# Optimization experiments

Hardware: AMD Instinct MI355X
Metric: run time of the kernel (lower is better)

## Reference

```python
import jax, jax.numpy as jnp
import numpy as np

N_STREAMS = 8
DIM = 1024
N_HEADS = 16
HEAD_DIM = DIM // N_HEADS
STREAM_DIM = DIM // N_STREAMS
EPS = 1e-6


def setup_inputs() -> dict:
    key = jax.random.key(0)
    ks = jax.random.split(key, 20)
    B, S, D = 2, 2048, DIM
    inp = {
        "x": jax.random.normal(ks[0], (B, S, D), jnp.float32),
        "rope_cos": jax.random.uniform(ks[1], (S, HEAD_DIM), jnp.float32),
        "rope_sin": jax.random.uniform(ks[2], (S, HEAD_DIM), jnp.float32),
        # DeltaOperator: learned per-channel decay logits
        "delta_decay": jax.random.normal(ks[3], (D,), jnp.float32) * 0.02,
        # gate_proj: Linear(D, 3*n)
        "gate_w": jax.random.normal(ks[4], (3 * N_STREAMS, D), jnp.float32) * 0.02,
        "gate_b": jnp.zeros((3 * N_STREAMS,), jnp.float32),
        "phi_res": jax.random.normal(ks[5], (N_STREAMS, N_STREAMS), jnp.float32) * 0.02,
        "ln1_w": jnp.ones((D,), jnp.float32),
        "ln2_w": jnp.ones((D,), jnp.float32),
        # MLP (StrategicLinear == Linear at inference)
        "w1": jax.random.normal(ks[6], (4 * D, D), jnp.float32) * 0.02,
        "b1": jnp.zeros((4 * D,), jnp.float32),
        "w2": jax.random.normal(ks[7], (D, 4 * D), jnp.float32) * 0.02,
        "b2": jnp.zeros((D,), jnp.float32),
        # nn.MultiheadAttention params
        "in_proj_w": jax.random.normal(ks[8], (3 * D, D), jnp.float32) * 0.02,
        "in_proj_b": jnp.zeros((3 * D,), jnp.float32),
        "out_w": jax.random.normal(ks[9], (D, D), jnp.float32) * 0.02,
        "out_b": jnp.zeros((D,), jnp.float32),
    }
    return inp


def delta_operator(x, decay_logits):
    # out_t = x_t - s_{t-1};  s_t = beta*s_{t-1} + (1-beta)*x_t  (per-channel EMA delta)
    beta = jax.nn.sigmoid(decay_logits)  # [D]

    def step(s, xt):
        out = xt - s
        s_new = beta * s + (1.0 - beta) * xt
        return s_new, out

    xT = jnp.swapaxes(x, 0, 1)  # [S,B,D]
    s0 = jnp.zeros_like(xT[0])
    _, ysT = jax.lax.scan(step, s0, xT)
    return jnp.swapaxes(ysT, 0, 1)  # [B,S,D]


def rms_norm(x, w):
    var = jnp.mean(x * x, axis=-1, keepdims=True)
    return x * jax.lax.rsqrt(var + EPS) * w


def sinkhorn_knopp(phi, iterations=15):
    K = jnp.exp(phi)
    for _ in range(iterations):
        K = K / jnp.sum(K, axis=1, keepdims=True)
        K = K / jnp.sum(K, axis=0, keepdims=True)
    return K


def causal_mha(x, in_proj_w, in_proj_b, out_w, out_b):
    B, S, D = x.shape
    qkv = x @ in_proj_w.T + in_proj_b  # [B,S,3D]
    q, k, v = jnp.split(qkv, 3, axis=-1)
    def heads(t):
        return t.reshape(B, S, N_HEADS, HEAD_DIM).transpose(0, 2, 1, 3)  # [B,H,S,hd]
    q, k, v = heads(q), heads(k), heads(v)
    scores = jnp.einsum("bhqd,bhkd->bhqk", q, k) / jnp.sqrt(jnp.float32(HEAD_DIM))
    mask = jnp.tril(jnp.ones((S, S), bool))
    scores = jnp.where(mask, scores, jnp.float32(-1e9))
    attn = jax.nn.softmax(scores, axis=-1)
    o = jnp.einsum("bhqk,bhkd->bhqd", attn, v)
    o = o.transpose(0, 2, 1, 3).reshape(B, S, D)
    return o @ out_w.T + out_b


def reference(x, rope_cos, rope_sin, delta_decay, gate_w, gate_b, phi_res,
              ln1_w, ln2_w, w1, b1, w2, b2, in_proj_w, in_proj_b, out_w, out_b):
    B, S, D = x.shape
    n = N_STREAMS
    x_delta = delta_operator(x, delta_decay)
    x_state = jnp.mean(x_delta, axis=1)  # [B,D]
    gates = x_state @ gate_w.T + gate_b  # [B,3n]
    g_res = jax.nn.sigmoid(gates[:, 2 * n:])[:, None, :, None]  # [B,1,n,1]
    H_res = sinkhorn_knopp(phi_res, 15)
    x_streams = x_delta.reshape(B, S, n, STREAM_DIM)
    # (x_perm @ H.T).permute back == einsum over stream axis
    mhc_out = jnp.einsum("bsnd,mn->bsmd", x_streams * g_res, H_res).reshape(B, S, D)
    normed = rms_norm(x_delta, ln1_w)
    attn_out = causal_mha(normed, in_proj_w, in_proj_b, out_w, out_b)
    normed2 = rms_norm(x_delta + attn_out, ln2_w)
    h = jax.nn.gelu(normed2 @ w1.T + b1, approximate=False)
    ffn_out = h @ w2.T + b2
    return x_delta + attn_out + ffn_out + mhc_out
```

## Files before the change

### kernel.cpp

```cpp
#include <hip/hip_runtime.h>
#include <hip/hip_bf16.h>
#include <math.h>

#define BB 2
#define SS 2048
#define DDIM 1024
#define NHEAD 16
#define NSTR 8
#define SDIMC 128
#define NCH 16
#define CLEN 128
#define EPSV 1e-6f

using bf16 = __hip_bfloat16;
typedef __attribute__((ext_vector_type(8))) __bf16 bf8;
typedef __attribute__((ext_vector_type(4))) __bf16 bf4v;
typedef __attribute__((ext_vector_type(4))) float f4;

__device__ __forceinline__ bf16 f2b(float v) { return __float2bfloat16(v); }
__device__ __forceinline__ bf8 ld8(const bf16* p) { return *(const bf8*)p; }
__device__ __forceinline__ f4 MFMA(bf8 a, bf8 b, f4 c) {
  return __builtin_amdgcn_mfma_f32_16x16x32_bf16(a, b, c, 0, 0, 0);
}
__device__ __forceinline__ float sigm(float x) { return 1.0f / (1.0f + expf(-x)); }
__device__ __forceinline__ float fexp2(float x) { return __builtin_amdgcn_exp2f(x); }
__device__ __forceinline__ float max3f(float a, float b, float c) {
  return fmaxf(fmaxf(a, b), c);
}

__device__ __forceinline__ float gelu_f(float v) {
  float x = v * 0.70710678118654752f;
  float ax = fabsf(x);
  float t = __builtin_amdgcn_rcpf(1.0f + 0.3275911f * ax);
  float p = ((((1.061405429f * t - 1.453152027f) * t + 1.421413741f) * t
              - 0.284496736f) * t + 0.254829592f) * t;
  float e = 1.0f - p * fexp2(-ax * ax * 1.4426950408889634f);
  e = copysignf(e, x);
  return 0.5f * v * (1.0f + e);
}

__device__ __forceinline__ void glds16(bf16* l, const bf16* g) {
  __builtin_amdgcn_global_load_lds(
      (const __attribute__((address_space(1))) unsigned int*)g,
      (__attribute__((address_space(3))) unsigned int*)l, 16, 0, 0);
}

__global__ __launch_bounds__(256) void cvt_all(const float* __restrict__ ipw,
                                               const float* __restrict__ ow,
                                               const float* __restrict__ w1,
                                               const float* __restrict__ w2,
                                               bf16* __restrict__ WIPW,
                                               bf16* __restrict__ WOW,
                                               bf16* __restrict__ W1B,
                                               bf16* __restrict__ W2B) {
  const int S1 = 3 * DDIM * DDIM, S2 = S1 + DDIM * DDIM,
            S3 = S2 + 4 * DDIM * DDIM;
  int i4 = (blockIdx.x * 256 + threadIdx.x) * 4;
  const float* src;
  bf16* dst;
  int off;
  if (i4 < S1)      { src = ipw; dst = WIPW; off = i4; }
  else if (i4 < S2) { src = ow;  dst = WOW;  off = i4 - S1; }
  else if (i4 < S3) { src = w1;  dst = W1B;  off = i4 - S2; }
  else              { src = w2;  dst = W2B;  off = i4 - S3; }
  float4 v = *(const float4*)(src + off);
  bf4v o;
  o[0] = (__bf16)v.x; o[1] = (__bf16)v.y; o[2] = (__bf16)v.z; o[3] = (__bf16)v.w;
  *(bf4v*)(dst + off) = o;
}

__global__ __launch_bounds__(256) void delta_passA(const float* __restrict__ x,
                                                   const float* __restrict__ decay,
                                                   float* __restrict__ SA) {
  int idx = blockIdx.x * 256 + threadIdx.x;
  int d = idx % DDIM;
  int c = (idx / DDIM) % NCH;
  int b = idx / (DDIM * NCH);
  float beta = sigm(decay[d]);
  float omb = 1.0f - beta;
  const float* xp = x + ((size_t)(b * SS + c * CLEN)) * DDIM + d;
  float s = 0.0f;
  for (int j = 0; j < CLEN; j++) {
    float xv = xp[(size_t)j * DDIM];
    s = beta * s + omb * xv;
  }
  SA[idx] = s;
}

__global__ __launch_bounds__(256) void delta_passB(const float* __restrict__ SA,
                                                   const float* __restrict__ decay,
                                                   float* __restrict__ SIN) {
  int idx = blockIdx.x * 256 + threadIdx.x;
  int d = idx % DDIM;
  int b = idx / DDIM;
  float beta = sigm(decay[d]);
  float p = beta;
  for (int i = 0; i < 7; i++) p *= p;
  float s = 0.0f;
  for (int c = 0; c < NCH; c++) {
    SIN[(b * NCH + c) * DDIM + d] = s;
    s = p * s + SA[(b * NCH + c) * DDIM + d];
  }
}

__global__ __launch_bounds__(256) void delta_passC(const float* __restrict__ x,
                                                   const float* __restrict__ decay,
                                                   const float* __restrict__ SIN,
                                                   float* __restrict__ XD,
                                                   float* __restrict__ SA) {
  int idx = blockIdx.x * 256 + threadIdx.x;
  int d = idx % DDIM;
  int c = (idx / DDIM) % NCH;
  int b = idx / (DDIM * NCH);
  float beta = sigm(decay[d]);
  float omb = 1.0f - beta;
  const float* xp = x + ((size_t)(b * SS + c * CLEN)) * DDIM + d;
  float* xdp = XD + ((size_t)(b * SS + c * CLEN)) * DDIM + d;
  float s = SIN[idx];
  float sum = 0.0f;
  for (int j = 0; j < CLEN; j++) {
    float xv = xp[(size_t)j * DDIM];
    float o = xv - s;
    xdp[(size_t)j * DDIM] = o;
    sum += o;
    s = beta * s + omb * xv;
  }
  SA[idx] = sum;
}

__global__ __launch_bounds__(1024) void gates_sinkhorn(const float* __restrict__ SA,
                                                       const float* __restrict__ gw,
                                                       const float* __restrict__ gb,
                                                       const float* __restrict__ phi,
                                                       float* __restrict__ gres,
                                                       float* __restrict__ hres) {
  int tid = threadIdx.x;
  int wave = tid >> 6, lane = tid & 63;
  int b = wave >> 3, j = wave & 7;
  float acc = 0.0f;
  for (int d = lane; d < DDIM; d += 64) {
    float xs = 0.0f;
    for (int c = 0; c < NCH; c++) xs += SA[(b * NCH + c) * DDIM + d];
    xs *= (1.0f / (float)SS);
    acc += xs * gw[(2 * NSTR + j) * DDIM + d];
  }
  for (int off = 32; off > 0; off >>= 1) acc += __shfl_down(acc, off);
  if (lane == 0) gres[b * NSTR + j] = sigm(acc + gb[2 * NSTR + j]);
  __syncthreads();
  if (tid == 0) {
    float Km[8][8];
    for (int i = 0; i < 8; i++)
      for (int jj = 0; jj < 8; jj++) Km[i][jj] = expf(phi[i * 8 + jj]);
    for (int it = 0; it < 15; it++) {
      for (int i = 0; i < 8; i++) {
        float rs = 0.0f;
        for (int jj = 0; jj < 8; jj++) rs += Km[i][jj];
        float inv = 1.0f / rs;
        for (int jj = 0; jj < 8; jj++) Km[i][jj] *= inv;
      }
      for (int jj = 0; jj < 8; jj++) {
        float cs = 0.0f;
        for (int i = 0; i < 8; i++) cs += Km[i][jj];
        float inv = 1.0f / cs;
        for (int i = 0; i < 8; i++) Km[i][jj] *= inv;
      }
    }
    for (int i = 0; i < 8; i++)
      for (int jj = 0; jj < 8; jj++) hres[i * 8 + jj] = Km[i][jj];
  }
}

__global__ __launch_bounds__(256) void rmsnorm_k(const float* __restrict__ in,
                                                 const float* __restrict__ w,
                                                 bf16* __restrict__ out) {
  int row = blockIdx.x;
  const float* r = in + (size_t)row * DDIM;
  int tid = threadIdx.x;
  float ss = 0.0f;
  for (int i = tid; i < DDIM; i += 256) {
    float v = r[i];
    ss += v * v;
  }
  for (int off = 32; off > 0; off >>= 1) ss += __shfl_down(ss, off);
  __shared__ float red[4];
  if ((tid & 63) == 0) red[tid >> 6] = ss;
  __syncthreads();
  float tot = red[0] + red[1] + red[2] + red[3];
  float sc = rsqrtf(tot / (float)DDIM + EPSV);
  bf16* o = out + (size_t)row * DDIM;
  for (int i = tid; i < DDIM; i += 256) o[i] = f2b(r[i] * sc * w[i]);
}

template <int EPI>
__global__ __launch_bounds__(512, 2) void gemm256(const bf16* __restrict__ Ag,
                                                  const bf16* __restrict__ Wg,
                                                  const float* __restrict__ bias,
                                                  bf16* __restrict__ outp,
                                                  int M, int N, int K, int nby) {
  __shared__ __align__(16) bf16 As[2][16384];
  __shared__ __align__(16) bf16 Bs[2][16384];
  int nwg = gridDim.x;
  int cpx = nwg >> 3;
  int l = (blockIdx.x & 7) * cpx + (blockIdx.x >> 3);
  int bm = l / nby, bn = l % nby;
  int m0 = bm * 256, n0 = bn * 256;
  int tid = threadIdx.x;
  int lane = tid & 63, wv = tid >> 6;
  int ml = lane & 15, quad = lane >> 4;
  int wrow = wv >> 2, wcol = wv & 3;

  size_t aoff[2][2], boff[2][2];
  int lof[2][2];
#pragma unroll
  for (int h = 0; h < 2; h++)
#pragma unroll
    for (int j = 0; j < 2; j++) {
      int b = tid * 16 + j * 8192;
      int s = b >> 10, w = b & 1023;
      int wl = w ^ (((w >> 9) & 1) << 5);
      int row = h * 128 + (s >> 1) * 16 + (wl >> 6);
      int col = (s & 1) * 32 + ((wl & 63) >> 1);
      aoff[h][j] = (size_t)(m0 + row) * K + col;
      boff[h][j] = (size_t)(n0 + row) * K + col;
      lof[h][j] = (h * 16384 + b) >> 1;
    }
  int wq2 = ((((ml << 6) + (quad << 4)) ^ (((int)(ml >= 8)) << 5))) >> 1;

#define SA_(c, kt, h) { glds16(&As[c][lof[h][0]], Ag + aoff[h][0] + (size_t)(kt) * 64); \
                        glds16(&As[c][lof[h][1]], Ag + aoff[h][1] + (size_t)(kt) * 64); }
#define SB_(c, kt, h) { glds16(&Bs[c][lof[h][0]], Wg + boff[h][0] + (size_t)(kt) * 64); \
                        glds16(&Bs[c][lof[h][1]], Wg + boff[h][1] + (size_t)(kt) * 64); }

  SA_(0, 0, 0); SA_(0, 0, 1);
  SB_(0, 0, 0); SB_(0, 0, 1);
  SB_(1, 1, 0); SB_(1, 1, 1);
  f4 acc[8][4] = {};
  asm volatile("s_waitcnt vmcnt(4)" ::: "memory");
  __builtin_amdgcn_s_barrier();
  asm volatile("" ::: "memory");

  int T = K >> 6;
  for (int t = 0; t < T; t++) {
    int c = t & 1;
    bf8 bfrag[4][2];
#pragma unroll
    for (int q = 0; q < 4; q++) {
      bf8 af[2][2];
#pragma unroll
      for (int mi2 = 0; mi2 < 2; mi2++)
#pragma unroll
        for (int kk = 0; kk < 2; kk++)
          af[mi2][kk] =
              ld8(&As[c][(((wrow * 8 + q * 2 + mi2) * 2 + kk) << 9) + wq2]);
      if (q == 0) {
#pragma unroll
        for (int ni = 0; ni < 4; ni++)
#pragma unroll
          for (int kk = 0; kk < 2; kk++)
            bfrag[ni][kk] =
                ld8(&Bs[c][(((wcol * 4 + ni) * 2 + kk) << 9) + wq2]);
      }
      if (q == 0 && t + 1 < T) SA_(c ^ 1, t + 1, 0);
      if (q == 1 && t + 1 < T) SA_(c ^ 1, t + 1, 1);
      if (q == 2 && t + 2 < T) SB_(c, t + 2, 0);
      if (q == 3 && t + 2 < T) SB_(c, t + 2, 1);
      __builtin_amdgcn_s_barrier();
      asm volatile("s_waitcnt lgkmcnt(0)" ::: "memory");
      __builtin_amdgcn_s_setprio(1);
#pragma unroll
      for (int mi2 = 0; mi2 < 2; mi2++)
#pragma unroll
        for (int ni = 0; ni < 4; ni++)
#pragma unroll
          for (int kk = 0; kk < 2; kk++)
            acc[q * 2 + mi2][ni] =
                MFMA(af[mi2][kk], bfrag[ni][kk], acc[q * 2 + mi2][ni]);
      __builtin_amdgcn_s_setprio(0);
      if (q == 3) {
        if (t + 2 < T) {
          asm volatile("s_waitcnt vmcnt(4)" ::: "memory");
        } else if (t + 1 < T) {
          asm volatile("s_waitcnt vmcnt(0)" ::: "memory");
        }
      }
      __builtin_amdgcn_s_barrier();
      asm volatile("" ::: "memory");
    }
  }
#pragma unroll
  for (int mi = 0; mi < 8; mi++)
#pragma unroll
    for (int ni = 0; ni < 4; ni++)
#pragma unroll
      for (int r = 0; r < 4; r++) {
        int row = m0 + wrow * 128 + mi * 16 + quad * 4 + r;
        int col = n0 + wcol * 64 + ni * 16 + ml;
        float v = acc[mi][ni][r] + bias[col];
        if (EPI == 1) v = gelu_f(v);
        outp[(size_t)row * N + col] = f2b(v);
      }
#undef SA_
#undef SB_
}

__global__ __launch_bounds__(512, 2) void gemm256sk(const bf16* __restrict__ Ag,
                                                    const bf16* __restrict__ Wg,
                                                    bf16* __restrict__ P01,
                                                    bf16* __restrict__ P23,
                                                    int M, int N, int K, int LDK,
                                                    int nby) {
  __shared__ __align__(16) bf16 As[2][16384];
  __shared__ __align__(16) bf16 Bs[2][16384];
  int nwg = gridDim.x;
  int cpx = nwg >> 3;
  int l = (blockIdx.x & 7) * cpx + (blockIdx.x >> 3);
  int nper = nwg >> 2;
  int sk = l / nper;
  int idx = l % nper;
  int bm = idx / nby, bn = idx % nby;
  int m0 = bm * 256, n0 = bn * 256;
  bf16* outp = (sk < 2) ? (P01 + (size_t)sk * M * N)
                        : (P23 + (size_t)(sk - 2) * M * N);
  int kbase = sk * K;
  int tid = threadIdx.x;
  int lane = tid & 63, wv = tid >> 6;
  int ml = lane & 15, quad = lane >> 4;
  int wrow = wv >> 2, wcol = wv & 3;

  size_t aoff[2][2], boff[2][2];
  int lof[2][2];
#pragma unroll
  for (int h = 0; h < 2; h++)
#pragma unroll
    for (int j = 0; j < 2; j++) {
      int b = tid * 16 + j * 8192;
      int s = b >> 10, w = b & 1023;
      int wl = w ^ (((w >> 9) & 1) << 5);
      int row = h * 128 + (s >> 1) * 16 + (wl >> 6);
      int col = (s & 1) * 32 + ((wl & 63) >> 1);
      aoff[h][j] = (size_t)(m0 + row) * LDK + kbase + col;
      boff[h][j] = (size_t)(n0 + row) * LDK + kbase + col;
      lof[h][j] = (h * 16384 + b) >> 1;
    }
  int wq2 = ((((ml << 6) + (quad << 4)) ^ (((int)(ml >= 8)) << 5))) >> 1;

#define SA_(c, kt, h) { glds16(&As[c][lof[h][0]], Ag + aoff[h][0] + (size_t)(kt) * 64); \
                        glds16(&As[c][lof[h][1]], Ag + aoff[h][1] + (size_t)(kt) * 64); }
#define SB_(c, kt, h) { glds16(&Bs[c][lof[h][0]], Wg + boff[h][0] + (size_t)(kt) * 64); \
                        glds16(&Bs[c][lof[h][1]], Wg + boff[h][1] + (size_t)(kt) * 64); }

  SA_(0, 0, 0); SA_(0, 0, 1);
  SB_(0, 0, 0); SB_(0, 0, 1);
  SB_(1, 1, 0); SB_(1, 1, 1);
  f4 acc[8][4] = {};
  asm volatile("s_waitcnt vmcnt(4)" ::: "memory");
  __builtin_amdgcn_s_barrier();
  asm volatile("" ::: "memory");

  int T = K >> 6;
  for (int t = 0; t < T; t++) {
    int c = t & 1;
    bf8 bfrag[4][2];
#pragma unroll
    for (int q = 0; q < 4; q++) {
      bf8 af[2][2];
#pragma unroll
      for (int mi2 = 0; mi2 < 2; mi2++)
#pragma unroll
        for (int kk = 0; kk < 2; kk++)
          af[mi2][kk] =
              ld8(&As[c][(((wrow * 8 + q * 2 + mi2) * 2 + kk) << 9) + wq2]);
      if (q == 0) {
#pragma unroll
        for (int ni = 0; ni < 4; ni++)
#pragma unroll
          for (int kk = 0; kk < 2; kk++)
            bfrag[ni][kk] =
                ld8(&Bs[c][(((wcol * 4 + ni) * 2 + kk) << 9) + wq2]);
      }
      if (q == 0 && t + 1 < T) SA_(c ^ 1, t + 1, 0);
      if (q == 1 && t + 1 < T) SA_(c ^ 1, t + 1, 1);
      if (q == 2 && t + 2 < T) SB_(c, t + 2, 0);
      if (q == 3 && t + 2 < T) SB_(c, t + 2, 1);
      __builtin_amdgcn_s_barrier();
      asm volatile("s_waitcnt lgkmcnt(0)" ::: "memory");
      __builtin_amdgcn_s_setprio(1);
#pragma unroll
      for (int mi2 = 0; mi2 < 2; mi2++)
#pragma unroll
        for (int ni = 0; ni < 4; ni++)
#pragma unroll
          for (int kk = 0; kk < 2; kk++)
            acc[q * 2 + mi2][ni] =
                MFMA(af[mi2][kk], bfrag[ni][kk], acc[q * 2 + mi2][ni]);
      __builtin_amdgcn_s_setprio(0);
      if (q == 3) {
        if (t + 2 < T) {
          asm volatile("s_waitcnt vmcnt(4)" ::: "memory");
        } else if (t + 1 < T) {
          asm volatile("s_waitcnt vmcnt(0)" ::: "memory");
        }
      }
      __builtin_amdgcn_s_barrier();
      asm volatile("" ::: "memory");
    }
  }
#pragma unroll
  for (int mi = 0; mi < 8; mi++)
#pragma unroll
    for (int ni = 0; ni < 4; ni++)
#pragma unroll
      for (int r = 0; r < 4; r++) {
        int row = m0 + wrow * 128 + mi * 16 + quad * 4 + r;
        int col = n0 + wcol * 64 + ni * 16 + ml;
        outp[(size_t)row * N + col] = f2b(acc[mi][ni][r]);
      }
#undef SA_
#undef SB_
}

template <int ODT, int EPI>
__global__ __launch_bounds__(256) void gemm_lds64(const bf16* __restrict__ A,
                                                  const bf16* __restrict__ W,
                                                  const float* __restrict__ bias,
                                                  const float* __restrict__ res,
                                                  void* __restrict__ outp,
                                                  int M, int N, int K) {
  __shared__ bf16 As[2][64 * 32];
  __shared__ bf16 Bs[2][128 * 32];
  int tid = threadIdx.x;
  int lane = tid & 63, wv = tid >> 6;
  int ml = lane & 15, quad = lane >> 4;
  int wr = wv & 1, wc = wv >> 1;
  int m0 = blockIdx.x * 64, n0 = blockIdx.y * 128;
  const bf16* gaA;
  const bf16* gb[2];
  int lofA, lofs[2];
  {
    int c = tid;
    int row = c >> 2, kc = (c & 3) * 8;
    gaA = A + (size_t)(m0 + row) * K + kc;
    lofA = c * 8;
  }
#pragma unroll
  for (int it = 0; it < 2; it++) {
    int c = it * 256 + tid;
    int row = c >> 2, kc = (c & 3) * 8;
    gb[it] = W + (size_t)(n0 + row) * K + kc;
    lofs[it] = c * 8;
  }
  glds16(&As[0][lofA], gaA);
#pragma unroll
  for (int it = 0; it < 2; it++) glds16(&Bs[0][lofs[it]], gb[it]);
  f4 acc[2][4] = {};
  int nk = K >> 5;
  int cur = 0;
  __syncthreads();
  for (int t = 0; t < nk; t++) {
    if (t + 1 < nk) {
      int ko = (t + 1) * 32;
      glds16(&As[cur ^ 1][lofA], gaA + ko);
#pragma unroll
      for (int it = 0; it < 2; it++) glds16(&Bs[cur ^ 1][lofs[it]], gb[it] + ko);
    }
    bf8 af[2], bfr[4];
#pragma unroll
    for (int mi = 0; mi < 2; mi++)
      af[mi] = ld8(&As[cur][(wr * 32 + mi * 16 + ml) * 32 + quad * 8]);
#pragma unroll
    for (int ni = 0; ni < 4; ni++)
      bfr[ni] = ld8(&Bs[cur][(wc * 64 + ni * 16 + ml) * 32 + quad * 8]);
#pragma unroll
    for (int mi = 0; mi < 2; mi++)
#pragma unroll
      for (int ni = 0; ni < 4; ni++)
        acc[mi][ni] = MFMA(af[mi], bfr[ni], acc[mi][ni]);
    __syncthreads();
    cur ^= 1;
  }
#pragma unroll
  for (int mi = 0; mi < 2; mi++)
#pragma unroll
    for (int ni = 0; ni < 4; ni++)
#pragma unroll
      for (int r = 0; r < 4; r++) {
        int row = m0 + wr * 32 + mi * 16 + quad * 4 + r;
        int col = n0 + wc * 64 + ni * 16 + ml;
        size_t idx = (size_t)row * N + col;
        float v = acc[mi][ni][r] + bias[col];
        if (EPI == 1) v = gelu_f(v);
        if (EPI == 2) v += res[idx];
        if (ODT == 1) ((bf16*)outp)[idx] = f2b(v);
        else ((float*)outp)[idx] = v;
      }
}

__global__ __launch_bounds__(256) void vtrans(const bf16* __restrict__ qkv,
                                              bf16* __restrict__ VT) {
  int bid = blockIdx.x;
  int st = bid % (SS / 64);
  int h = (bid / (SS / 64)) % NHEAD;
  int b = bid / ((SS / 64) * NHEAD);
  __shared__ bf16 tile[64][65];
  int s0 = st * 64;
  int tid = threadIdx.x;
  for (int it = 0; it < 16; it++) {
    int sl = it * 4 + (tid >> 6), dl = tid & 63;
    tile[sl][dl] = qkv[(size_t)(b * SS + s0 + sl) * (3 * DDIM) + 2 * DDIM + h * 64 + dl];
  }
  __syncthreads();
  for (int it = 0; it < 16; it++) {
    int dl = it * 4 + (tid >> 6), sl = tid & 63;
    VT[((size_t)(b * NHEAD + h) * 64 + dl) * SS + s0 + sl] = tile[sl][dl];
  }
}

__device__ __forceinline__ void qk_softmax(int kt, int q0, int nkt,
                                           const bf8 kf[4][2], const bf8* qf,
                                           f4* oacc, float& m, float& l,
                                           bf8* pf, bf16 (*pl)[72],
                                           int ml, int quad, int k0) {
  const float SC = 0.125f * 1.44269504089f;
  f4 s[4] = {{0,0,0,0},{0,0,0,0},{0,0,0,0},{0,0,0,0}};
  __builtin_amdgcn_s_setprio(1);
#pragma unroll
  for (int kk = 0; kk < 2; kk++)
#pragma unroll
    for (int c = 0; c < 4; c++)
      s[c] = MFMA(kf[c][kk], qf[kk], s[c]);
  __builtin_amdgcn_s_setprio(0);
  if (kt == nkt - 1) {
    int qi = q0 + ml;
#pragma unroll
    for (int c = 0; c < 4; c++)
#pragma unroll
      for (int r = 0; r < 4; r++)
        if (k0 + c * 16 + quad * 4 + r > qi) s[c][r] = -1e30f;
  }
  float mx = max3f(s[0][0], s[0][1], s[0][2]);
  mx = max3f(mx, s[0][3], s[1][0]);
  mx = max3f(mx, s[1][1], s[1][2]);
  mx = max3f(mx, s[1][3], s[2][0]);
  mx = max3f(mx, s[2][1], s[2][2]);
  mx = max3f(mx, s[2][3], s[3][0]);
  mx = max3f(mx, s[3][1], s[3][2]);
  mx = fmaxf(mx, s[3][3]);
  mx = fmaxf(mx, __shfl_xor(mx, 16));
  mx = fmaxf(mx, __shfl_xor(mx, 32));
  float mxs = mx * SC;
  float p[4][4];
  float rs = 0.0f;
  if (__all(mxs - m <= 8.0f)) {
#pragma unroll
    for (int c = 0; c < 4; c++)
#pragma unroll
      for (int r = 0; r < 4; r++) {
        p[c][r] = fexp2(__builtin_fmaf(s[c][r], SC, -m));
        rs += p[c][r];
      }
    rs += __shfl_xor(rs, 16);
    rs += __shfl_xor(rs, 32);
    l += rs;
  } else {
    float mn = fmaxf(m, mxs);
    float alpha = fexp2(m - mn);
#pragma unroll
    for (int c = 0; c < 4; c++)
#pragma unroll
      for (int r = 0; r < 4; r++) {
        p[c][r] = fexp2(__builtin_fmaf(s[c][r], SC, -mn));
        rs += p[c][r];
      }
    rs += __shfl_xor(rs, 16);
    rs += __shfl_xor(rs, 32);
    l = l * alpha + rs;
    m = mn;
    float alr[4];
#pragma unroll
    for (int r = 0; r < 4; r++) alr[r] = __shfl(alpha, quad * 4 + r);
#pragma unroll
    for (int c = 0; c < 4; c++)
#pragma unroll
      for (int r = 0; r < 4; r++) oacc[c][r] *= alr[r];
  }
#pragma unroll
  for (int c = 0; c < 4; c++) {
    bf4v w;
#pragma unroll
    for (int r = 0; r < 4; r++) w[r] = (__bf16)p[c][r];
    *(bf4v*)&pl[ml][c * 16 + quad * 4] = w;
  }
#pragma unroll
  for (int kk = 0; kk < 2; kk++) pf[kk] = ld8(&pl[ml][kk * 32 + quad * 8]);
}

__global__ __launch_bounds__(512, 4) void flash_attn(const bf16* __restrict__ qkv,
                                                     const bf16* __restrict__ VT,
                                                     bf16* __restrict__ obuf) {
  int rb = blockIdx.x;
  int slot = rb >> 3;
  int bid = (rb & 7) * 64 + slot;
  int j = slot & 15;
  int blk = (slot & 32) ? (15 - j) : j;
  int h = (bid >> 4) & 15;
  int b = bid >> 8;
  int tid = threadIdx.x;
  int wv = tid >> 6, lane = tid & 63;
  int ml = lane & 15, quad = lane >> 4;
  int half = wv >> 2, sub = wv & 3;
  int idx = half ? (127 - (blk * 4 + sub)) : (blk * 4 + sub);
  int q0 = idx * 16;
  int nkt = half ? (32 - blk) : (blk + 1);
  int maxn = 32 - blk;

  __shared__ __align__(16) bf16 Ks[2][64 * 64];
  __shared__ __align__(16) bf16 Vs[2][64 * 64];
  __shared__ __align__(16) bf16 plds[8][16][72];
  bf16 (*pl)[72] = plds[wv];

  bf8 qf[2];
#pragma unroll
  for (int kk = 0; kk < 2; kk++)
    qf[kk] = ld8(qkv + (size_t)(b * SS + q0 + ml) * (3 * DDIM) + h * 64 + kk * 32 + quad * 8);
  f4 oacc[4] = {{0,0,0,0},{0,0,0,0},{0,0,0,0},{0,0,0,0}};
  float m = -1e30f, l = 0.0f;

  const bf16* kglob = qkv + (size_t)b * SS * (3 * DDIM) + DDIM + h * 64;
  const bf16* vglob = VT + (size_t)(b * NHEAD + h) * 64 * SS;

  {
    int lam = tid;
    int row = lam >> 3;
    int ch = (lam & 7) ^ (row & 7);
    glds16(&Ks[0][lam * 8], kglob + (size_t)row * (3 * DDIM) + ch * 8);
    glds16(&Vs[0][lam * 8], vglob + (size_t)row * SS + ch * 8);
  }
  __syncthreads();
  int cur = 0;
  for (int kt = 0; kt < maxn; kt++) {
    int k0 = kt * 64;
    if (kt + 1 < maxn) {
      int k0n = (kt + 1) * 64;
      int lam = tid;
      int row = lam >> 3;
      int ch = (lam & 7) ^ (row & 7);
      glds16(&Ks[cur ^ 1][lam * 8], kglob + (size_t)(k0n + row) * (3 * DDIM) + ch * 8);
      glds16(&Vs[cur ^ 1][lam * 8], vglob + (size_t)row * SS + k0n + ch * 8);
    }
    if (kt < nkt) {
      bf8 kf[4][2];
#pragma unroll
      for (int kk = 0; kk < 2; kk++)
#pragma unroll
        for (int c = 0; c < 4; c++) {
          int chunk = ((c * 16 + ml) << 3) + ((kk * 4 + quad) ^ (ml & 7));
          kf[c][kk] = ld8(&Ks[cur][chunk * 8]);
        }
      bf8 pf[2];
      qk_softmax(kt, q0, nkt, kf, qf, oacc, m, l, pf, pl, ml, quad, k0);
      bf8 vf[4][2];
#pragma unroll
      for (int kk = 0; kk < 2; kk++)
#pragma unroll
        for (int c = 0; c < 4; c++) {
          int chunk = ((c * 16 + ml) << 3) + ((kk * 4 + quad) ^ (ml & 7));
          vf[c][kk] = ld8(&Vs[cur][chunk * 8]);
        }
      __builtin_amdgcn_s_setprio(1);
#pragma unroll
      for (int c = 0; c < 4; c++)
#pragma unroll
        for (int kk = 0; kk < 2; kk++)
          oacc[c] = MFMA(pf[kk], vf[c][kk], oacc[c]);
      __builtin_amdgcn_s_setprio(0);
    }
    __syncthreads();
    cur ^= 1;
  }
  float ln[4];
#pragma unroll
  for (int r = 0; r < 4; r++) ln[r] = __shfl(l, quad * 4 + r);
#pragma unroll
  for (int c = 0; c < 4; c++)
#pragma unroll
    for (int r = 0; r < 4; r++) {
      int row = q0 + quad * 4 + r;
      obuf[(size_t)(b * SS + row) * DDIM + h * 64 + c * 16 + ml] =
          f2b(oacc[c][r] / ln[r]);
    }
}

__global__ __launch_bounds__(256) void final_k(const float* __restrict__ y,
                                               const bf16* __restrict__ P0,
                                               const bf16* __restrict__ P1,
                                               const bf16* __restrict__ P2,
                                               const bf16* __restrict__ P3,
                                               const float* __restrict__ bias,
                                               const float* __restrict__ xd,
                                               const float* __restrict__ hres,
                                               const float* __restrict__ gres,
                                               float* __restrict__ out) {
  int row = blockIdx.x;
  int b = row / SS;
  int tid = threadIdx.x;
  __shared__ float cf[8][8];
  if (tid < 64) cf[tid >> 3][tid & 7] = hres[tid] * gres[b * NSTR + (tid & 7)];
  __syncthreads();
  int i4 = tid * 4;
  int m = i4 >> 7, dd = i4 & 127;
  size_t base = (size_t)row * DDIM + i4;
  f4 vy = *(const f4*)(y + base);
  f4 vb = *(const f4*)(bias + i4);
  bf4v p0 = *(const bf4v*)(P0 + base);
  bf4v p1 = *(const bf4v*)(P1 + base);
  bf4v p2 = *(const bf4v*)(P2 + base);
  bf4v p3 = *(const bf4v*)(P3 + base);
  const float* xr = xd + (size_t)row * DDIM;
  float acc[4];
#pragma unroll
  for (int jj = 0; jj < 4; jj++)
    acc[jj] = vy[jj] + vb[jj] + (float)p0[jj] + (float)p1[jj] +
              (float)p2[jj] + (float)p3[jj];
#pragma unroll
  for (int n = 0; n < 8; n++) {
    f4 vx = *(const f4*)(xr + n * SDIMC + dd);
#pragma unroll
    for (int jj = 0; jj < 4; jj++) acc[jj] += cf[m][n] * vx[jj];
  }
  f4 vo = {acc[0], acc[1], acc[2], acc[3]};
  *(f4*)(out + base) = vo;
}

extern "C" void kernel_launch(void* const* d_in, const int* in_sizes, int n_in,
                              void* d_out, int out_size, void* d_ws, size_t ws_size,
                              hipStream_t stream) {
  const float* x     = (const float*)d_in[0];
  const float* decay = (const float*)d_in[3];
  const float* gw    = (const float*)d_in[4];
  const float* gb    = (const float*)d_in[5];
  const float* phi   = (const float*)d_in[6];
  const float* ln1   = (const float*)d_in[7];
  const float* ln2   = (const float*)d_in[8];
  const float* w1    = (const float*)d_in[9];
  const float* b1    = (const float*)d_in[10];
  const float* w2    = (const float*)d_in[11];
  const float* b2    = (const float*)d_in[12];
  const float* ipw   = (const float*)d_in[13];
  const float* ipb   = (const float*)d_in[14];
  const float* ow    = (const float*)d_in[15];
  const float* obs   = (const float*)d_in[16];
  float* out = (float*)d_out;

  const size_t MB = 1048576ull;
  char* wsp = (char*)d_ws;
  float* SA   = (float*)(wsp);
  float* SIN  = (float*)(wsp + 131072ull);
  float* GRES = (float*)(wsp + 262144ull);
  float* HRES = (float*)(wsp + 262208ull);
  float* XD   = (float*)(wsp + 1 * MB);
  float* AO   = (float*)(wsp + 17 * MB);
  bf16*  NORM = (bf16*)(wsp + 33 * MB);
  bf16*  OB   = (bf16*)(wsp + 41 * MB);
  bf16*  QKV  = (bf16*)(wsp + 49 * MB);
  bf16*  VT   = (bf16*)(wsp + 73 * MB);
  bf16*  HB   = (bf16*)(wsp + 49 * MB);
  bf16*  WIPW = (bf16*)(wsp + 81 * MB);
  bf16*  WOW  = (bf16*)(wsp + 87 * MB);
  bf16*  W1B  = (bf16*)(wsp + 89 * MB);
  bf16*  W2B  = (bf16*)(wsp + 97 * MB);
  bf16* PKB0 = (bf16*)(wsp + 33 * MB);
  bf16* PKB2 = (bf16*)(wsp + 81 * MB);

  cvt_all<<<dim3(12 * DDIM * DDIM / 1024), dim3(256), 0, stream>>>(
      ipw, ow, w1, w2, WIPW, WOW, W1B, W2B);

  delta_passA<<<dim3(BB * NCH * DDIM / 256), dim3(256), 0, stream>>>(x, decay, SA);
  delta_passB<<<dim3(BB * DDIM / 256), dim3(256), 0, stream>>>(SA, decay, SIN);
  delta_passC<<<dim3(BB * NCH * DDIM / 256), dim3(256), 0, stream>>>(x, decay, SIN, XD, SA);
  gates_sinkhorn<<<dim3(1), dim3(1024), 0, stream>>>(SA, gw, gb, phi, GRES, HRES);
  rmsnorm_k<<<dim3(BB * SS), dim3(256), 0, stream>>>(XD, ln1, NORM);
  gemm256<0><<<dim3(192), dim3(512), 0, stream>>>(NORM, WIPW, ipb, QKV,
                                                  BB * SS, 3 * DDIM, DDIM, 12);
  vtrans<<<dim3(BB * NHEAD * (SS / 64)), dim3(256), 0, stream>>>(QKV, VT);
  flash_attn<<<dim3(BB * NHEAD * 16), dim3(512), 0, stream>>>(QKV, VT, OB);
  gemm_lds64<0, 2><<<dim3(64, 8), dim3(256), 0, stream>>>(OB, WOW, obs, XD,
                                                          AO, BB * SS, DDIM, DDIM);
  rmsnorm_k<<<dim3(BB * SS), dim3(256), 0, stream>>>(AO, ln2, NORM);
  gemm256<1><<<dim3(256), dim3(512), 0, stream>>>(NORM, W1B, b1, HB,
                                                  BB * SS, 4 * DDIM, DDIM, 16);
  gemm256sk<<<dim3(256), dim3(512), 0, stream>>>(HB, W2B, PKB0, PKB2,
                                                 BB * SS, DDIM, DDIM, 4 * DDIM, 4);
  final_k<<<dim3(BB * SS), dim3(256), 0, stream>>>(
      AO, PKB0, PKB0 + (size_t)BB * SS * DDIM, PKB2,
      PKB2 + (size_t)BB * SS * DDIM, b2, XD, HRES, GRES, out);
}
```

Baseline: 402.1 us.

## Replace 256x256 pipelined GEMM with simpler 128x128 double-buffered GEMM for QKV and FFN1

```diff
diff --git a/kernel.cpp b/kernel.cpp
--- a/kernel.cpp
+++ b/kernel.cpp
@@ -191,116 +191,79 @@
   for (int i = tid; i < DDIM; i += 256) o[i] = f2b(r[i] * sc * w[i]);
 }
 
-template <int EPI>
-__global__ __launch_bounds__(512, 2) void gemm256(const bf16* __restrict__ Ag,
-                                                  const bf16* __restrict__ Wg,
-                                                  const float* __restrict__ bias,
-                                                  bf16* __restrict__ outp,
-                                                  int M, int N, int K, int nby) {
-  __shared__ __align__(16) bf16 As[2][16384];
-  __shared__ __align__(16) bf16 Bs[2][16384];
-  int nwg = gridDim.x;
-  int cpx = nwg >> 3;
-  int l = (blockIdx.x & 7) * cpx + (blockIdx.x >> 3);
-  int bm = l / nby, bn = l % nby;
-  int m0 = bm * 256, n0 = bn * 256;
+template <int ODT, int EPI>
+__global__ __launch_bounds__(256) void gemm_lds(const bf16* __restrict__ A,
+                                                const bf16* __restrict__ W,
+                                                const float* __restrict__ bias,
+                                                const float* __restrict__ res,
+                                                void* __restrict__ outp,
+                                                int M, int N, int K) {
+  __shared__ bf16 As[2][128 * 32];
+  __shared__ bf16 Bs[2][128 * 32];
   int tid = threadIdx.x;
   int lane = tid & 63, wv = tid >> 6;
   int ml = lane & 15, quad = lane >> 4;
-  int wrow = wv >> 2, wcol = wv & 3;
-
-  size_t aoff[2][2], boff[2][2];
-  int lof[2][2];
-#pragma unroll
-  for (int h = 0; h < 2; h++)
-#pragma unroll
-    for (int j = 0; j < 2; j++) {
-      int b = tid * 16 + j * 8192;
-      int s = b >> 10, w = b & 1023;
-      int wl = w ^ (((w >> 9) & 1) << 5);
-      int row = h * 128 + (s >> 1) * 16 + (wl >> 6);
-      int col = (s & 1) * 32 + ((wl & 63) >> 1);
-      aoff[h][j] = (size_t)(m0 + row) * K + col;
-      boff[h][j] = (size_t)(n0 + row) * K + col;
-      lof[h][j] = (h * 16384 + b) >> 1;
+  int wr = wv >> 1, wc = wv & 1;
+  int m0 = blockIdx.x * 128, n0 = blockIdx.y * 128;
+  const bf16* ga[2];
+  const bf16* gb[2];
+  int lofs[2];
+#pragma unroll
+  for (int it = 0; it < 2; it++) {
+    int c = it * 256 + tid;
+    int row = c >> 2, kc = (c & 3) * 8;
+    ga[it] = A + (size_t)(m0 + row) * K + kc;
+    gb[it] = W + (size_t)(n0 + row) * K + kc;
+    lofs[it] = c * 8;
+  }
+#pragma unroll
+  for (int it = 0; it < 2; it++) {
+    glds16(&As[0][lofs[it]], ga[it]);
+    glds16(&Bs[0][lofs[it]], gb[it]);
+  }
+  f4 acc[4][4] = {};
+  int nk = K >> 5;
+  int cur = 0;
+  __syncthreads();
+  for (int t = 0; t < nk; t++) {
+    if (t + 1 < nk) {
+      int ko = (t + 1) * 32;
+#pragma unroll
+      for (int it = 0; it < 2; it++) {
+        glds16(&As[cur ^ 1][lofs[it]], ga[it] + ko);
+        glds16(&Bs[cur ^ 1][lofs[it]], gb[it] + ko);
+      }
     }
-  int wq2 = ((((ml << 6) + (quad << 4)) ^ (((int)(ml >= 8)) << 5))) >> 1;
-
-#define SA_(c, kt, h) { glds16(&As[c][lof[h][0]], Ag + aoff[h][0] + (size_t)(kt) * 64); \
-                        glds16(&As[c][lof[h][1]], Ag + aoff[h][1] + (size_t)(kt) * 64); }
-#define SB_(c, kt, h) { glds16(&Bs[c][lof[h][0]], Wg + boff[h][0] + (size_t)(kt) * 64); \
-                        glds16(&Bs[c][lof[h][1]], Wg + boff[h][1] + (size_t)(kt) * 64); }
-
-  SA_(0, 0, 0); SA_(0, 0, 1);
-  SB_(0, 0, 0); SB_(0, 0, 1);
-  SB_(1, 1, 0); SB_(1, 1, 1);
-  f4 acc[8][4] = {};
-  asm volatile("s_waitcnt vmcnt(4)" ::: "memory");
-  __builtin_amdgcn_s_barrier();
-  asm volatile("" ::: "memory");
-
-  int T = K >> 6;
-  for (int t = 0; t < T; t++) {
-    int c = t & 1;
-    bf8 bfrag[4][2];
-#pragma unroll
-    for (int q = 0; q < 4; q++) {
-      bf8 af[2][2];
-#pragma unroll
-      for (int mi2 = 0; mi2 < 2; mi2++)
-#pragma unroll
-        for (int kk = 0; kk < 2; kk++)
-          af[mi2][kk] =
-              ld8(&As[c][(((wrow * 8 + q * 2 + mi2) * 2 + kk) << 9) + wq2]);
-      if (q == 0) {
-#pragma unroll
-        for (int ni = 0; ni < 4; ni++)
-#pragma unroll
-          for (int kk = 0; kk < 2; kk++)
-            bfrag[ni][kk] =
-                ld8(&Bs[c][(((wcol * 4 + ni) * 2 + kk) << 9) + wq2]);
-      }
-      if (q == 0 && t + 1 < T) SA_(c ^ 1, t + 1, 0);
-      if (q == 1 && t + 1 < T) SA_(c ^ 1, t + 1, 1);
-      if (q == 2 && t + 2 < T) SB_(c, t + 2, 0);
-      if (q == 3 && t + 2 < T) SB_(c, t + 2, 1);
-      __builtin_amdgcn_s_barrier();
-      asm volatile("s_waitcnt lgkmcnt(0)" ::: "memory");
-      __builtin_amdgcn_s_setprio(1);
-#pragma unroll
-      for (int mi2 = 0; mi2 < 2; mi2++)
-#pragma unroll
-        for (int ni = 0; ni < 4; ni++)
-#pragma unroll
-          for (int kk = 0; kk < 2; kk++)
-            acc[q * 2 + mi2][ni] =
-                MFMA(af[mi2][kk], bfrag[ni][kk], acc[q * 2 + mi2][ni]);
-      __builtin_amdgcn_s_setprio(0);
-      if (q == 3) {
-        if (t + 2 < T) {
-          asm volatile("s_waitcnt vmcnt(4)" ::: "memory");
-        } else if (t + 1 < T) {
-          asm volatile("s_waitcnt vmcnt(0)" ::: "memory");
-        }
-      }
-      __builtin_amdgcn_s_barrier();
-      asm volatile("" ::: "memory");
-    }
-  }
-#pragma unroll
-  for (int mi = 0; mi < 8; mi++)
+    bf8 af[4], bfr[4];
+#pragma unroll
+    for (int mi = 0; mi < 4; mi++)
+      af[mi] = ld8(&As[cur][(wr * 64 + mi * 16 + ml) * 32 + quad * 8]);
 #pragma unroll
     for (int ni = 0; ni < 4; ni++)
+      bfr[ni] = ld8(&Bs[cur][(wc * 64 + ni * 16 + ml) * 32 + quad * 8]);
+#pragma unroll
+    for (int mi = 0; mi < 4; mi++)
+#pragma unroll
+      for (int ni = 0; ni < 4; ni++)
+        acc[mi][ni] = MFMA(af[mi], bfr[ni], acc[mi][ni]);
+    __syncthreads();
+    cur ^= 1;
+  }
+#pragma unroll
+  for (int mi = 0; mi < 4; mi++)
+#pragma unroll
+    for (int ni = 0; ni < 4; ni++)
 #pragma unroll
       for (int r = 0; r < 4; r++) {
-        int row = m0 + wrow * 128 + mi * 16 + quad * 4 + r;
-        int col = n0 + wcol * 64 + ni * 16 + ml;
+        int row = m0 + wr * 64 + mi * 16 + quad * 4 + r;
+        int col = n0 + wc * 64 + ni * 16 + ml;
+        size_t idx = (size_t)row * N + col;
         float v = acc[mi][ni][r] + bias[col];
         if (EPI == 1) v = gelu_f(v);
-        outp[(size_t)row * N + col] = f2b(v);
-      }
-#undef SA_
-#undef SB_
+        if (EPI == 2) v += res[idx];
+        if (ODT == 1) ((bf16*)outp)[idx] = f2b(v);
+        else ((float*)outp)[idx] = v;
+      }
 }
 
 __global__ __launch_bounds__(512, 2) void gemm256sk(const bf16* __restrict__ Ag,
@@ -779,15 +742,15 @@
   delta_passC<<<dim3(BB * NCH * DDIM / 256), dim3(256), 0, stream>>>(x, decay, SIN, XD, SA);
   gates_sinkhorn<<<dim3(1), dim3(1024), 0, stream>>>(SA, gw, gb, phi, GRES, HRES);
   rmsnorm_k<<<dim3(BB * SS), dim3(256), 0, stream>>>(XD, ln1, NORM);
-  gemm256<0><<<dim3(192), dim3(512), 0, stream>>>(NORM, WIPW, ipb, QKV,
-                                                  BB * SS, 3 * DDIM, DDIM, 12);
+  gemm_lds<1, 0><<<dim3(32, 24), dim3(256), 0, stream>>>(NORM, WIPW, ipb, nullptr,
+                                                         QKV, BB * SS, 3 * DDIM, DDIM);
   vtrans<<<dim3(BB * NHEAD * (SS / 64)), dim3(256), 0, stream>>>(QKV, VT);
   flash_attn<<<dim3(BB * NHEAD * 16), dim3(512), 0, stream>>>(QKV, VT, OB);
   gemm_lds64<0, 2><<<dim3(64, 8), dim3(256), 0, stream>>>(OB, WOW, obs, XD,
                                                           AO, BB * SS, DDIM, DDIM);
   rmsnorm_k<<<dim3(BB * SS), dim3(256), 0, stream>>>(AO, ln2, NORM);
-  gemm256<1><<<dim3(256), dim3(512), 0, stream>>>(NORM, W1B, b1, HB,
-                                                  BB * SS, 4 * DDIM, DDIM, 16);
+  gemm_lds<1, 1><<<dim3(32, 32), dim3(256), 0, stream>>>(NORM, W1B, b1, nullptr,
+                                                         HB, BB * SS, 4 * DDIM, DDIM);
   gemm256sk<<<dim3(256), dim3(512), 0, stream>>>(HB, W2B, PKB0, PKB2,
                                                  BB * SS, DDIM, DDIM, 4 * DDIM, 4);
   final_k<<<dim3(BB * SS), dim3(256), 0, stream>>>(
```

After: 403.4 us. About the same (+0.3%).
